# Performance work log

Measured on AMD Instinct MI355X. Metric: run time of the kernel, lower is better.

## Reference

```python
import jax, jax.numpy as jnp
import numpy as np

EPS = 0.1  # self.eps in the torch module


def setup_inputs() -> dict:
    key = jax.random.key(0)
    k1, k2, k3, k4 = jax.random.split(key, 4)
    B, T, N = 16, 8192, 128
    # mel-energy style non-negative input
    x = jax.random.uniform(k1, (B, T, N), dtype=jnp.float32)
    # faithful parameter initializations from __init__
    log_alpha = jnp.log(jax.random.normal(k2, (N,), dtype=jnp.float32) * 0.1 + 1.0)
    log_delta = jnp.log(jax.random.normal(k3, (N,), dtype=jnp.float32) * 0.1 + 2.0)
    log_rho = jnp.log(jax.random.normal(k4, (N,), dtype=jnp.float32) * 0.1 + 0.6)
    sr, t, hop_size = 22050.0, 0.395, 512.0
    log_sigma = jnp.array([1.0 - np.exp(-hop_size / (t * sr))], dtype=jnp.float32)
    return {"x": x, "log_alpha": log_alpha, "log_delta": log_delta,
            "log_rho": log_rho, "log_sigma": log_sigma}


def reference(x, log_alpha, log_delta, log_rho, log_sigma):
    # x: [B, T, N]
    sigma = jnp.exp(log_sigma)[0]  # scalar smoothing coefficient

    def ema_step(m_prev, x_t):  # m_prev, x_t: [B, N]
        m_t = sigma * x_t + (1.0 - sigma) * m_prev
        return m_t, m_t

    B, T, N = x.shape
    m0 = jnp.zeros((B, N), dtype=x.dtype)  # torch code starts from zeros (m[:, -1] == 0 at t=0)
    _, m = jax.lax.scan(ema_step, m0, jnp.swapaxes(x, 0, 1))  # m: [T, B, N]
    m = jnp.swapaxes(m, 0, 1)  # [B, T, N]

    alpha = jnp.exp(log_alpha)  # [N], broadcasts over B, T
    delta = jnp.exp(log_delta)
    rho = jnp.exp(log_rho)
    pcen_out = (x / (m + EPS) ** alpha + delta) ** rho - delta ** rho
    return pcen_out
```

## Files before the change

### kernel.cpp

```cpp
#include <hip/hip_runtime.h>
#include <cmath>


constexpr int S    = 16;
constexpr int K    = 8;
constexpr int ROWS = 4;

__global__ __launch_bounds__(256, 4)
void pcen_kernel(const float* __restrict__ x,
                 const float* __restrict__ log_alpha,
                 const float* __restrict__ log_delta,
                 const float* __restrict__ log_rho,
                 const float* __restrict__ log_sigma,
                 float* __restrict__ out,
                 int T, int N)
{
    const int tid  = threadIdx.x;
    const int lane = tid & 63;
    const int row  = tid >> 6;
    const int n2   = lane * 2;
    const int b    = blockIdx.y;
    const int t0   = (blockIdx.x * ROWS + row) * S;

    const size_t base = ((size_t)b * T + t0) * (size_t)N + n2;
    const float* px = x   + base;
    float*       po = out + base;

    float2 w[K];
    float2 v[S];
    if (t0 > 0) {
        const float* pw = px - (size_t)K * N;
        #pragma unroll
        for (int j = 0; j < K; ++j) w[j] = *(const float2*)(pw + (size_t)j * N);
    }
    #pragma unroll
    for (int j = 0; j < S; ++j) v[j] = *(const float2*)(px + (size_t)j * N);

    float2 la = *(const float2*)(log_alpha + n2);
    float2 ld = *(const float2*)(log_delta + n2);
    float2 lr = *(const float2*)(log_rho   + n2);
    const float sigma = expf(log_sigma[0]);
    const float aa    = 1.0f - sigma;

    const float nax = -expf(la.x), nay = -expf(la.y);
    const float dx  =  expf(ld.x), dy  =  expf(ld.y);
    const float rx  =  expf(lr.x), ry  =  expf(lr.y);
    const float dpx = exp2f(rx * log2f(dx));
    const float dpy = exp2f(ry * log2f(dy));

    float mx = 0.0f, my = 0.0f;
    if (t0 > 0) {
        #pragma unroll
        for (int j = 0; j < K; ++j) {
            mx = fmaf(aa, mx, sigma * w[j].x);
            my = fmaf(aa, my, sigma * w[j].y);
        }
    }

    #pragma unroll
    for (int j = 0; j < S; ++j) {
        mx = fmaf(aa, mx, sigma * v[j].x);
        my = fmaf(aa, my, sigma * v[j].y);
        float2 ov;
        ov.x = exp2f(rx * log2f(fmaf(v[j].x,
                   exp2f(nax * log2f(mx + 0.1f)), dx))) - dpx;
        ov.y = exp2f(ry * log2f(fmaf(v[j].y,
                   exp2f(nay * log2f(my + 0.1f)), dy))) - dpy;
        *(float2*)(po + (size_t)j * N) = ov;
    }
}

extern "C" void kernel_launch(void* const* d_in, const int* in_sizes, int n_in,
                              void* d_out, int out_size, void* d_ws, size_t ws_size,
                              hipStream_t stream)
{
    const float* x  = (const float*)d_in[0];
    const float* la = (const float*)d_in[1];
    const float* ld = (const float*)d_in[2];
    const float* lr = (const float*)d_in[3];
    const float* ls = (const float*)d_in[4];
    float* out = (float*)d_out;

    const int N = in_sizes[1];
    const int T = 8192;
    const int B = in_sizes[0] / (T * N);

    dim3 grid(T / (S * ROWS), B);
    pcen_kernel<<<grid, 256, 0, stream>>>(x, la, ld, lr, ls, out, T, N);
}
```

Measured before the change: 120.9 us.

## Split tile loads into two halves, use raw hardware exp2/log, raise occupancy

Each thread now loads its 16-row tile in two chunks of 8, issuing the second chunk's loads after the warm-up EMA and before the first chunk is processed. Fewer live registers let the launch bound request 8 waves per SIMD instead of 4. The libm exp2f/log2f calls are replaced by __builtin_amdgcn_exp2f/logf, which skip the denormal and range fixups. Those builtins trade some accuracy and edge-case handling for fewer instructions, and the staged loads may expose more memory latency per wave.

New measurement: 122.5 us. About the same (+1.3%).

```diff
diff --git a/kernel.cpp b/kernel.cpp
--- a/kernel.cpp
+++ b/kernel.cpp
@@ -5,8 +5,9 @@
 constexpr int S    = 16;
 constexpr int K    = 8;
 constexpr int ROWS = 4;
+constexpr int C    = 8;
 
-__global__ __launch_bounds__(256, 4)
+__global__ __launch_bounds__(256, 8)
 void pcen_kernel(const float* __restrict__ x,
                  const float* __restrict__ log_alpha,
                  const float* __restrict__ log_delta,
@@ -27,14 +28,14 @@
     float*       po = out + base;
 
     float2 w[K];
-    float2 v[S];
+    float2 vA[C], vB[C];
     if (t0 > 0) {
         const float* pw = px - (size_t)K * N;
         #pragma unroll
         for (int j = 0; j < K; ++j) w[j] = *(const float2*)(pw + (size_t)j * N);
     }
     #pragma unroll
-    for (int j = 0; j < S; ++j) v[j] = *(const float2*)(px + (size_t)j * N);
+    for (int j = 0; j < C; ++j) vA[j] = *(const float2*)(px + (size_t)j * N);
 
     float2 la = *(const float2*)(log_alpha + n2);
     float2 ld = *(const float2*)(log_delta + n2);
@@ -45,8 +46,8 @@
     const float nax = -expf(la.x), nay = -expf(la.y);
     const float dx  =  expf(ld.x), dy  =  expf(ld.y);
     const float rx  =  expf(lr.x), ry  =  expf(lr.y);
-    const float dpx = exp2f(rx * log2f(dx));
-    const float dpy = exp2f(ry * log2f(dy));
+    const float dpx = __builtin_amdgcn_exp2f(rx * __builtin_amdgcn_logf(dx));
+    const float dpy = __builtin_amdgcn_exp2f(ry * __builtin_amdgcn_logf(dy));
 
     float mx = 0.0f, my = 0.0f;
     if (t0 > 0) {
@@ -58,15 +59,38 @@
     }
 
     #pragma unroll
-    for (int j = 0; j < S; ++j) {
-        mx = fmaf(aa, mx, sigma * v[j].x);
-        my = fmaf(aa, my, sigma * v[j].y);
+    for (int j = 0; j < C; ++j) vB[j] = *(const float2*)(px + (size_t)(C + j) * N);
+
+    #pragma unroll
+    for (int j = 0; j < C; ++j) {
+        mx = fmaf(aa, mx, sigma * vA[j].x);
+        my = fmaf(aa, my, sigma * vA[j].y);
         float2 ov;
-        ov.x = exp2f(rx * log2f(fmaf(v[j].x,
-                   exp2f(nax * log2f(mx + 0.1f)), dx))) - dpx;
-        ov.y = exp2f(ry * log2f(fmaf(v[j].y,
-                   exp2f(nay * log2f(my + 0.1f)), dy))) - dpy;
+        ov.x = __builtin_amdgcn_exp2f(rx * __builtin_amdgcn_logf(
+                   fmaf(vA[j].x,
+                        __builtin_amdgcn_exp2f(nax * __builtin_amdgcn_logf(mx + 0.1f)),
+                        dx))) - dpx;
+        ov.y = __builtin_amdgcn_exp2f(ry * __builtin_amdgcn_logf(
+                   fmaf(vA[j].y,
+                        __builtin_amdgcn_exp2f(nay * __builtin_amdgcn_logf(my + 0.1f)),
+                        dy))) - dpy;
         *(float2*)(po + (size_t)j * N) = ov;
+    }
+
+    #pragma unroll
+    for (int j = 0; j < C; ++j) {
+        mx = fmaf(aa, mx, sigma * vB[j].x);
+        my = fmaf(aa, my, sigma * vB[j].y);
+        float2 ov;
+        ov.x = __builtin_amdgcn_exp2f(rx * __builtin_amdgcn_logf(
+                   fmaf(vB[j].x,
+                        __builtin_amdgcn_exp2f(nax * __builtin_amdgcn_logf(mx + 0.1f)),
+                        dx))) - dpx;
+        ov.y = __builtin_amdgcn_exp2f(ry * __builtin_amdgcn_logf(
+                   fmaf(vB[j].y,
+                        __builtin_amdgcn_exp2f(nay * __builtin_amdgcn_logf(my + 0.1f)),
+                        dy))) - dpy;
+        *(float2*)(po + (size_t)(C + j) * N) = ov;
     }
 }
 
```

## Vectorize to float4, use raw exp2/log intrinsics, and stage loads in halves

Applied to the files above, without the earlier changes.

Each thread now handles four channels with float4 loads and stores, with eight time strips per block. The strip's second half is loaded into the reused halo registers after the halo warm-up, which lowers register pressure. All exp and log calls go to the AMDGCN hardware exp2/log builtins, skipping the library wrappers' range and denormal handling. This trades exact libm semantics for fewer instructions per element.

Result: no change. 122.2 us (+1.0%).

```diff
diff --git a/kernel.cpp b/kernel.cpp
--- a/kernel.cpp
+++ b/kernel.cpp
@@ -2,9 +2,13 @@
 #include <cmath>
 
 
-constexpr int S    = 16;
-constexpr int K    = 8;
-constexpr int ROWS = 4;
+constexpr int S  = 16;
+constexpr int K  = 8;
+constexpr int C  = 8;
+constexpr int SPB = 8;
+
+#define E2 __builtin_amdgcn_exp2f
+#define L2 __builtin_amdgcn_logf
 
 __global__ __launch_bounds__(256, 4)
 void pcen_kernel(const float* __restrict__ x,
@@ -15,58 +19,85 @@
                  float* __restrict__ out,
                  int T, int N)
 {
-    const int tid  = threadIdx.x;
-    const int lane = tid & 63;
-    const int row  = tid >> 6;
-    const int n2   = lane * 2;
-    const int b    = blockIdx.y;
-    const int t0   = (blockIdx.x * ROWS + row) * S;
+    const int tid   = threadIdx.x;
+    const int quad  = tid & 31;
+    const int strip = tid >> 5;
+    const int b     = blockIdx.y;
+    const int t0    = (blockIdx.x * SPB + strip) * S;
+    const int N4    = N >> 2;
 
-    const size_t base = ((size_t)b * T + t0) * (size_t)N + n2;
-    const float* px = x   + base;
-    float*       po = out + base;
+    const float4* px = (const float4*)x   + ((size_t)b * T + t0) * N4 + quad;
+    float4*       po = (float4*)out       + ((size_t)b * T + t0) * N4 + quad;
 
-    float2 w[K];
-    float2 v[S];
-    if (t0 > 0) {
-        const float* pw = px - (size_t)K * N;
+    float4 vA[C], vB[C];
+    const bool has_halo = (t0 > 0);
+    if (has_halo) {
+        const float4* pw = px - (size_t)K * N4;
         #pragma unroll
-        for (int j = 0; j < K; ++j) w[j] = *(const float2*)(pw + (size_t)j * N);
+        for (int j = 0; j < K; ++j) vA[j] = pw[(size_t)j * N4];
     }
     #pragma unroll
-    for (int j = 0; j < S; ++j) v[j] = *(const float2*)(px + (size_t)j * N);
+    for (int j = 0; j < C; ++j) vB[j] = px[(size_t)j * N4];
 
-    float2 la = *(const float2*)(log_alpha + n2);
-    float2 ld = *(const float2*)(log_delta + n2);
-    float2 lr = *(const float2*)(log_rho   + n2);
-    const float sigma = expf(log_sigma[0]);
+    const float LOG2E = 1.442695040888963f;
+    float4 la = ((const float4*)log_alpha)[quad];
+    float4 ld = ((const float4*)log_delta)[quad];
+    float4 lr = ((const float4*)log_rho)[quad];
+    const float sigma = E2(log_sigma[0] * LOG2E);
     const float aa    = 1.0f - sigma;
 
-    const float nax = -expf(la.x), nay = -expf(la.y);
-    const float dx  =  expf(ld.x), dy  =  expf(ld.y);
-    const float rx  =  expf(lr.x), ry  =  expf(lr.y);
-    const float dpx = exp2f(rx * log2f(dx));
-    const float dpy = exp2f(ry * log2f(dy));
+    float4 na, dl, rh, dp;
+    na.x = -E2(la.x * LOG2E); na.y = -E2(la.y * LOG2E);
+    na.z = -E2(la.z * LOG2E); na.w = -E2(la.w * LOG2E);
+    dl.x =  E2(ld.x * LOG2E); dl.y =  E2(ld.y * LOG2E);
+    dl.z =  E2(ld.z * LOG2E); dl.w =  E2(ld.w * LOG2E);
+    rh.x =  E2(lr.x * LOG2E); rh.y =  E2(lr.y * LOG2E);
+    rh.z =  E2(lr.z * LOG2E); rh.w =  E2(lr.w * LOG2E);
+    dp.x =  E2(rh.x * L2(dl.x)); dp.y = E2(rh.y * L2(dl.y));
+    dp.z =  E2(rh.z * L2(dl.z)); dp.w = E2(rh.w * L2(dl.w));
 
-    float mx = 0.0f, my = 0.0f;
-    if (t0 > 0) {
+    float4 m = make_float4(0.f, 0.f, 0.f, 0.f);
+    if (has_halo) {
         #pragma unroll
         for (int j = 0; j < K; ++j) {
-            mx = fmaf(aa, mx, sigma * w[j].x);
-            my = fmaf(aa, my, sigma * w[j].y);
+            m.x = fmaf(aa, m.x, sigma * vA[j].x);
+            m.y = fmaf(aa, m.y, sigma * vA[j].y);
+            m.z = fmaf(aa, m.z, sigma * vA[j].z);
+            m.w = fmaf(aa, m.w, sigma * vA[j].w);
         }
     }
 
     #pragma unroll
-    for (int j = 0; j < S; ++j) {
-        mx = fmaf(aa, mx, sigma * v[j].x);
-        my = fmaf(aa, my, sigma * v[j].y);
-        float2 ov;
-        ov.x = exp2f(rx * log2f(fmaf(v[j].x,
-                   exp2f(nax * log2f(mx + 0.1f)), dx))) - dpx;
-        ov.y = exp2f(ry * log2f(fmaf(v[j].y,
-                   exp2f(nay * log2f(my + 0.1f)), dy))) - dpy;
-        *(float2*)(po + (size_t)j * N) = ov;
+    for (int j = 0; j < C; ++j) vA[j] = px[(size_t)(C + j) * N4];
+
+    #pragma unroll
+    for (int j = 0; j < C; ++j) {
+        const float4 v = vB[j];
+        float4 o;
+        m.x = fmaf(aa, m.x, sigma * v.x);
+        m.y = fmaf(aa, m.y, sigma * v.y);
+        m.z = fmaf(aa, m.z, sigma * v.z);
+        m.w = fmaf(aa, m.w, sigma * v.w);
+        o.x = E2(rh.x * L2(fmaf(v.x, E2(na.x * L2(m.x + 0.1f)), dl.x))) - dp.x;
+        o.y = E2(rh.y * L2(fmaf(v.y, E2(na.y * L2(m.y + 0.1f)), dl.y))) - dp.y;
+        o.z = E2(rh.z * L2(fmaf(v.z, E2(na.z * L2(m.z + 0.1f)), dl.z))) - dp.z;
+        o.w = E2(rh.w * L2(fmaf(v.w, E2(na.w * L2(m.w + 0.1f)), dl.w))) - dp.w;
+        po[(size_t)j * N4] = o;
+    }
+
+    #pragma unroll
+    for (int j = 0; j < C; ++j) {
+        const float4 v = vA[j];
+        float4 o;
+        m.x = fmaf(aa, m.x, sigma * v.x);
+        m.y = fmaf(aa, m.y, sigma * v.y);
+        m.z = fmaf(aa, m.z, sigma * v.z);
+        m.w = fmaf(aa, m.w, sigma * v.w);
+        o.x = E2(rh.x * L2(fmaf(v.x, E2(na.x * L2(m.x + 0.1f)), dl.x))) - dp.x;
+        o.y = E2(rh.y * L2(fmaf(v.y, E2(na.y * L2(m.y + 0.1f)), dl.y))) - dp.y;
+        o.z = E2(rh.z * L2(fmaf(v.z, E2(na.z * L2(m.z + 0.1f)), dl.z))) - dp.z;
+        o.w = E2(rh.w * L2(fmaf(v.w, E2(na.w * L2(m.w + 0.1f)), dl.w))) - dp.w;
+        po[(size_t)(C + j) * N4] = o;
     }
 }
 
@@ -85,6 +116,6 @@
     const int T = 8192;
     const int B = in_sizes[0] / (T * N);
 
-    dim3 grid(T / (S * ROWS), B);
+    dim3 grid(T / (S * SPB), B);
     pcen_kernel<<<grid, 256, 0, stream>>>(x, la, ld, lr, ls, out, T, N);
 }
```
